# Kernel optimization log

Measured on AMD Instinct MI355X. Metric: run time of the kernel, lower is better.

## Reference

```python
import jax, jax.numpy as jnp
from jax import lax
import numpy as np
import math

B, C, Hs, Ws = 2, 512, 48, 48
HW = Hs * Ws            # 2304; also m (compress_ratio = 1)
M = HW
GROUPS = 256
GS = M // GROUPS        # 9, exact split
ALPHA = 0.05
MAXITER = 43
TOL = B * HW * 1e-7     # torch: z0.numel()*tol with z0 of shape [N, HW]
EPS = 1e-5
POWER_ITERS = 100


def _make_A():
    # random projection: num_ones = round(sqrt(m)) ones per column, rows L2-normalized
    rng = np.random.RandomState(0)
    num_ones = int(round(math.sqrt(M)))  # 48
    A = np.zeros((M, HW), dtype=np.float32)
    rows = np.argsort(rng.rand(HW, M), axis=1)[:, :num_ones]  # [HW, num_ones]
    A[rows.ravel(), np.repeat(np.arange(HW), num_ones)] = 1.0
    A /= np.maximum(np.sqrt((A ** 2).sum(axis=1, keepdims=True)), 1e-12)
    return jnp.asarray(A)


def setup_inputs() -> dict:
    key = jax.random.key(0)
    ks = jax.random.split(key, 10)
    f32 = jnp.float32
    d = {
        'content': jax.random.normal(ks[0], (B, C, Hs, Ws), f32),
        'style': jax.random.normal(ks[1], (B, C, Hs, Ws), f32),
        'content_key': jax.random.normal(ks[2], (B, C, Hs, Ws), f32),
        'style_key': jax.random.normal(ks[3], (B, C, Hs, Ws), f32),
        'f_w': jax.random.normal(ks[4], (C, C), f32) * 0.02,
        'f_b': jnp.zeros((C,), f32),
        'g_w': jax.random.normal(ks[5], (C, C), f32) * 0.02,
        'g_b': jnp.zeros((C,), f32),
        'h_w': jax.random.normal(ks[6], (C, C), f32) * 0.02,
        'h_b': jnp.zeros((C,), f32),
        'A': _make_A(),
    }
    return d


def _conv1x1(x, w, b):
    # nn.Conv2d(Cin, Cout, 1): [b,c,h,w] x [o,c] + bias
    return jnp.einsum('bchw,oc->bohw', x, w) + b[None, :, None, None]


def _softshrink(x, lam):
    return jnp.sign(x) * jnp.maximum(jnp.abs(x) - lam, 0.0)


def _forward(content, style, content_key, style_key, f_w, f_b, g_w, g_b, h_w, h_b, A):
    Fq = _conv1x1(content_key, f_w, f_b).reshape(B, C, HW).transpose(0, 2, 1)  # [b,HWc,Ck]
    G = _conv1x1(style_key, g_w, g_b).reshape(B, C, HW)                        # [b,Ck,HWs]
    Hh = _conv1x1(style, h_w, h_b).reshape(B, C, HW)
    # HW <= max_sample: no subsampling branch
    style_flat = Hh.transpose(0, 2, 1)                                         # [b,HWs,C]
    S = jax.nn.softmax(jnp.einsum('bqc,bck->bqk', Fq, G), axis=-1)             # [b,HWc,HWs]
    mean = jnp.einsum('bqk,bkc->bqc', S, style_flat)                           # weighted mean
    std = jnp.sqrt(jax.nn.relu(jnp.einsum('bqk,bkc->bqc', S, style_flat ** 2) - mean ** 2))
    mean = mean.transpose(0, 2, 1)  # [b,C,HW]
    std = std.transpose(0, 2, 1)
    # random projection along spatial dim: feat @ A^T
    proj = lambda f: jnp.einsum('mh,bch->bcm', A, f)
    mean_c = proj(mean)
    std_c = proj(std)
    cont_c = proj(content.reshape(B, C, HW))
    # per-group mean/variance norm (256 equal groups of GS along compressed dim)
    g = cont_c.reshape(B, C, GROUPS, GS)
    mu = g.mean(axis=-1, keepdims=True)
    var = g.var(axis=-1, ddof=1, keepdims=True)  # torch var is unbiased
    normed = (g - mu) / jnp.sqrt(var + EPS)
    x = (normed * std_c.reshape(B, C, GROUPS, GS)
         + mean_c.reshape(B, C, GROUPS, GS)).reshape(B, C, M)
    # FISTA sparse coding: min 0.5||z A^T - x||^2 + alpha |z|_1
    Ad = lax.stop_gradient(A)
    WtW = Ad.T @ Ad
    v = jnp.full((HW,), 1.0 / math.sqrt(HW), jnp.float32)
    def _pi(v, _):
        w = WtW @ v
        return w / jnp.linalg.norm(w), None
    v, _ = lax.scan(_pi, v, None, length=POWER_ITERS)
    L = v @ (WtW @ v)  # largest eigenvalue of A^T A
    lr = 1.0 / L
    z0 = jnp.zeros((B, C, HW), x.dtype)

    def step(carry, _):
        z, y, t, done = carry
        resid = jnp.einsum('bch,mh->bcm', y, A) - x   # y @ A^T - x
        grad = jnp.einsum('bcm,mh->bch', resid, A)    # resid @ A
        zn = _softshrink(y - lr * grad, ALPHA * lr)
        diff = jnp.abs(z - zn).sum()
        tn = (1.0 + jnp.sqrt(1.0 + 4.0 * t * t)) / 2.0
        yn = zn + (t - 1.0) / tn * (zn - z)
        z2 = jnp.where(done, z, zn)
        y2 = jnp.where(done, y, yn)
        t2 = jnp.where(done, t, tn)
        done2 = done | (diff <= TOL)
        return (z2, y2, t2, done2), None

    (z, _, _, _), _ = lax.scan(step, (z0, z0, jnp.float32(1.0), jnp.array(False)),
                               None, length=MAXITER)
    return z.reshape(B, C, Hs, Ws)


def reference(content, style, content_key, style_key, f_w, f_b, g_w, g_b, h_w, h_b, A):
    return _forward(content, style, content_key, style_key,
                    f_w, f_b, g_w, g_b, h_w, h_b, A)
```

## Files before the change

### kernel.cpp

```cpp
#include <hip/hip_runtime.h>
#include <math.h>

#define TPB 256

typedef _Float16 f16;
typedef _Float16 half8 __attribute__((ext_vector_type(8)));
typedef _Float16 f16x2 __attribute__((ext_vector_type(2)));
typedef _Float16 f16x4 __attribute__((ext_vector_type(4)));
typedef float floatx4 __attribute__((ext_vector_type(4)));

static constexpr int CDIM = 512;
static constexpr int HWD = 2304;
static constexpr float ALPHA = 0.05f;
static constexpr float TOLF = 4.608e-4f;

enum { EPI_F32 = 0, EPI_F16BIASN = 1, EPI_F16BIASM = 2, EPI_F16 = 3,
       EPI_WTW = 4, EPI_MEANSTD = 5, EPI_FISTA = 6 };

__device__ __forceinline__ bool fista_done(const float* __restrict__ diffArr, int iter) {
    bool done = false;
    for (int j = 0; j < iter; ++j) done = done || (diffArr[j] <= TOLF);
    return done;
}

__device__ __forceinline__ void gload_lds(const f16* g, f16* l) {
#if __has_builtin(__builtin_amdgcn_global_load_lds)
    __builtin_amdgcn_global_load_lds(
        (__attribute__((address_space(1))) void*)(g),
        (__attribute__((address_space(3))) void*)(l), 16, 0, 0);
#else
    *(int4*)l = *(const int4*)g;
#endif
}

template<int EPI, int MF>
__global__ __launch_bounds__(TPB, 3) void sgemm(
    const f16* __restrict__ A, long a_bs, int lda,
    const f16* __restrict__ B, long b_bs, int ldb,
    void* __restrict__ C0, long c_bs, int ldc,
    void* __restrict__ C1,
    int K,
    const float* __restrict__ bias,
    const float* __restrict__ xAf,
    float* __restrict__ zf, float* __restrict__ yf, f16* __restrict__ yhp,
    const float* __restrict__ lrs, float coef,
    float* __restrict__ diffArr, int iter)
{
    if (EPI == EPI_FISTA) {
        if (iter > 0 && fista_done(diffArr, iter)) return;
    }
    __shared__ alignas(16) f16 As[MF * 32 * 64];
    __shared__ alignas(16) f16 Bs[64 * 64];
    const int tid = threadIdx.x;
    const int wid = tid >> 6, lane = tid & 63;
    const int wr = wid >> 1, wc = wid & 1;
    const int m0 = blockIdx.y * (MF * 32), n0 = blockIdx.x << 6;
    const f16* Ab = A + (long)blockIdx.z * a_bs;
    const f16* Bb = B + (long)blockIdx.z * b_bs;

    floatx4 acc[MF][2] = {};
    floatx4 acc2[MF][2] = {};

    const int rl = lane & 15, kg = lane >> 4;
    const int lrow = lane >> 3;
    const int gs = (lane & 7) ^ lrow;

    for (int k0 = 0; k0 < K; k0 += 64) {
        #pragma unroll
        for (int p = 0; p < MF; ++p) {
            const int c = wid * MF + p;
            const int R = c * 8 + lrow;
            gload_lds(Ab + (long)(m0 + R) * lda + k0 + gs * 8, &As[c * 512]);
        }
        #pragma unroll
        for (int p = 0; p < 2; ++p) {
            const int c = wid * 2 + p;
            const int R = c * 8 + lrow;
            gload_lds(Bb + (long)(n0 + R) * ldb + k0 + gs * 8, &Bs[c * 512]);
        }
        __syncthreads();
        #pragma unroll
        for (int kk = 0; kk < 2; ++kk) {
            const int j = kk * 4 + kg;
            half8 af[MF], bf[2];
            #pragma unroll
            for (int f = 0; f < MF; ++f) {
                const int rowa = wr * (MF * 16) + f * 16 + rl;
                af[f] = *(const half8*)&As[rowa * 64 + ((j ^ (rowa & 7)) * 8)];
            }
            #pragma unroll
            for (int f = 0; f < 2; ++f) {
                const int rowb = wc * 32 + f * 16 + rl;
                bf[f] = *(const half8*)&Bs[rowb * 64 + ((j ^ (rowb & 7)) * 8)];
            }
            #pragma unroll
            for (int fi = 0; fi < MF; ++fi) {
                #pragma unroll
                for (int fj = 0; fj < 2; ++fj) {
                    acc[fi][fj] = __builtin_amdgcn_mfma_f32_16x16x32_f16(af[fi], bf[fj], acc[fi][fj], 0, 0, 0);
                    if constexpr (EPI == EPI_MEANSTD) {
                        half8 bq = bf[fj] * bf[fj];
                        acc2[fi][fj] = __builtin_amdgcn_mfma_f32_16x16x32_f16(af[fi], bq, acc2[fi][fj], 0, 0, 0);
                    }
                }
            }
        }
        __syncthreads();
    }

    const int rg = lane >> 4;
    const int bz = blockIdx.z;
    float loc = 0.f;
    float lr = 0.f, sh = 0.f;
    if constexpr (EPI == EPI_FISTA) { lr = lrs[0]; sh = lrs[1]; }

    #pragma unroll
    for (int fi = 0; fi < MF; ++fi) {
        #pragma unroll
        for (int fj = 0; fj < 2; ++fj) {
            #pragma unroll
            for (int r = 0; r < 4; ++r) {
                const int row = m0 + wr * (MF * 16) + fi * 16 + rg * 4 + r;
                const int col = n0 + wc * 32 + fj * 16 + rl;
                const float v = acc[fi][fj][r];
                if constexpr (EPI == EPI_F32) {
                    ((float*)C0)[bz * c_bs + (long)row * ldc + col] = v;
                } else if constexpr (EPI == EPI_F16BIASN) {
                    ((f16*)C0)[bz * c_bs + (long)row * ldc + col] = (f16)(v + bias[col]);
                } else if constexpr (EPI == EPI_F16BIASM) {
                    ((f16*)C0)[bz * c_bs + (long)row * ldc + col] = (f16)(v + bias[row]);
                } else if constexpr (EPI == EPI_F16) {
                    ((f16*)C0)[bz * c_bs + (long)row * ldc + col] = (f16)v;
                } else if constexpr (EPI == EPI_WTW) {
                    ((float*)C0)[(long)row * ldc + col] = v;
                    ((f16*)C1)[(long)row * ldc + col] = (f16)v;
                } else if constexpr (EPI == EPI_MEANSTD) {
                    const float m_ = v;
                    float s2 = acc2[fi][fj][r] - m_ * m_;
                    const long o = ((long)bz * CDIM + col) * HWD + row;
                    ((f16*)C0)[o] = (f16)m_;
                    ((f16*)C1)[o] = (f16)sqrtf(s2 > 0.f ? s2 : 0.f);
                } else {
                    const long off = (long)row * HWD + col;
                    const float grad = v - xAf[off];
                    const float zo = zf[off];
                    const float p = yf[off] - lr * grad;
                    const float ap = fabsf(p) - sh;
                    const float zn = ap > 0.f ? copysignf(ap, p) : 0.f;
                    zf[off] = zn;
                    const float yn = zn + coef * (zn - zo);
                    yf[off] = yn;
                    yhp[off] = (f16)yn;
                    loc += fabsf(zn - zo);
                }
            }
        }
    }
    if constexpr (EPI == EPI_FISTA) {
        __shared__ float red[TPB];
        red[tid] = loc; __syncthreads();
        for (int s = 128; s > 0; s >>= 1) { if (tid < s) red[tid] += red[tid + s]; __syncthreads(); }
        if (tid == 0) atomicAdd(&diffArr[iter], red[0]);
    }
}

__global__ __launch_bounds__(TPB) void tcvt(const float* __restrict__ in, long in_bs,
                                            f16* __restrict__ out, long out_bs, int R, int Cc) {
    __shared__ float t[32][33];
    const int b = blockIdx.z;
    const int r0 = blockIdx.y << 5, c0 = blockIdx.x << 5;
    const int tx = threadIdx.x & 31, ty = threadIdx.x >> 5;
    const float* ib = in + (long)b * in_bs;
    #pragma unroll
    for (int p = 0; p < 4; ++p) {
        const int r = ty + p * 8;
        t[r][tx] = ib[(long)(r0 + r) * Cc + c0 + tx];
    }
    __syncthreads();
    f16* ob = out + (long)b * out_bs;
    #pragma unroll
    for (int p = 0; p < 4; ++p) {
        const int c = ty + p * 8;
        ob[(long)(c0 + c) * R + r0 + tx] = (f16)t[tx][c];
    }
}

__global__ void cvt16(const float4* __restrict__ in, f16x4* __restrict__ out, long n4) {
    long i = (long)blockIdx.x * blockDim.x + threadIdx.x;
    const long st = (long)gridDim.x * blockDim.x;
    for (; i < n4; i += st) {
        const float4 v = in[i];
        f16x4 o; o.x = (f16)v.x; o.y = (f16)v.y; o.z = (f16)v.z; o.w = (f16)v.w;
        out[i] = o;
    }
}

__global__ __launch_bounds__(TPB) void softmax_h(const float* __restrict__ Sf, f16* __restrict__ Sh) {
    __shared__ float row[HWD];
    __shared__ float red[TPB];
    const long base = (long)blockIdx.x * HWD;
    const int tid = threadIdx.x;
    float mx = -3.4e38f;
    for (int i = tid; i < HWD; i += TPB) { const float v = Sf[base + i]; row[i] = v; mx = fmaxf(mx, v); }
    red[tid] = mx; __syncthreads();
    for (int s = 128; s > 0; s >>= 1) { if (tid < s) red[tid] = fmaxf(red[tid], red[tid + s]); __syncthreads(); }
    mx = red[0]; __syncthreads();
    float sum = 0.f;
    for (int i = tid; i < HWD; i += TPB) { const float e = expf(row[i] - mx); row[i] = e; sum += e; }
    red[tid] = sum; __syncthreads();
    for (int s = 128; s > 0; s >>= 1) { if (tid < s) red[tid] += red[tid + s]; __syncthreads(); }
    const float inv = 1.0f / red[0];
    for (int i = tid; i < HWD; i += TPB) Sh[base + i] = (f16)(row[i] * inv);
}

__global__ __launch_bounds__(TPB) void groupnorm_x(const float* __restrict__ contc,
                                                   const float* __restrict__ meanc,
                                                   const float* __restrict__ stdc,
                                                   f16* __restrict__ xh) {
    const long base = (long)blockIdx.x * HWD + (long)threadIdx.x * 9;
    float v[9];
    float mu = 0.f;
    #pragma unroll
    for (int j = 0; j < 9; ++j) { v[j] = contc[base + j]; mu += v[j]; }
    mu *= (1.0f / 9.0f);
    float var = 0.f;
    #pragma unroll
    for (int j = 0; j < 9; ++j) { const float d = v[j] - mu; var += d * d; }
    var *= (1.0f / 8.0f);
    const float rs = 1.0f / sqrtf(var + 1e-5f);
    #pragma unroll
    for (int j = 0; j < 9; ++j)
        xh[base + j] = (f16)((v[j] - mu) * rs * (float)stdc[base + j] + (float)meanc[base + j]);
}

__global__ __launch_bounds__(TPB) void matvec_h(const f16* __restrict__ Wm,
                                                const float* __restrict__ win,
                                                float* __restrict__ wout) {
    __shared__ float red[TPB];
    const int tid = threadIdx.x;
    float s = 0.f;
    for (int i = tid; i < HWD; i += TPB) { const float v = win[i]; s += v * v; }
    red[tid] = s; __syncthreads();
    for (int st = 128; st > 0; st >>= 1) { if (tid < st) red[tid] += red[tid + st]; __syncthreads(); }
    const float ninv = rsqrtf(red[0]);
    const int row = (blockIdx.x << 2) + (tid >> 6);
    const int lane = tid & 63;
    const f16x2* wr2 = (const f16x2*)(Wm + (long)row * HWD);
    float d = 0.f;
    for (int j = lane; j < HWD / 2; j += 64) {
        const f16x2 p = wr2[j];
        d += (float)p.x * win[2 * j] + (float)p.y * win[2 * j + 1];
    }
    #pragma unroll
    for (int o = 32; o > 0; o >>= 1) d += __shfl_down(d, o);
    if (lane == 0) wout[row] = d * ninv;
}

__global__ __launch_bounds__(TPB) void kernelL(const float* __restrict__ Wf,
                                               const float* __restrict__ w,
                                               float* __restrict__ Lnum, float* __restrict__ Lden) {
    __shared__ float red[TPB];
    const int tid = threadIdx.x;
    const int row = (blockIdx.x << 2) + (tid >> 6);
    const int lane = tid & 63;
    const float* wr = Wf + (long)row * HWD;
    float d = 0.f;
    for (int j = lane; j < HWD; j += 64) d += wr[j] * w[j];
    #pragma unroll
    for (int o = 32; o > 0; o >>= 1) d += __shfl_down(d, o);
    red[tid] = (lane == 0) ? d * w[row] : 0.f;
    __syncthreads();
    for (int s = 128; s > 0; s >>= 1) { if (tid < s) red[tid] += red[tid + s]; __syncthreads(); }
    if (tid == 0) atomicAdd(Lnum, red[0]);
    if (blockIdx.x == 0) {
        __syncthreads();
        float s2 = 0.f;
        for (int i = tid; i < HWD; i += TPB) { const float v = w[i]; s2 += v * v; }
        red[tid] = s2; __syncthreads();
        for (int s = 128; s > 0; s >>= 1) { if (tid < s) red[tid] += red[tid + s]; __syncthreads(); }
        if (tid == 0) *Lden = red[0];
    }
}

__global__ void lr_fin(const float* __restrict__ Lnum, const float* __restrict__ Lden,
                       float* __restrict__ lrs) {
    const float lr = Lden[0] / Lnum[0];
    lrs[0] = lr;
    lrs[1] = ALPHA * lr;
}

__global__ void init_small(float* __restrict__ wvec, float* __restrict__ diffArr,
                           float* __restrict__ Lnum) {
    const int tid = threadIdx.x;
    for (int i = tid; i < HWD; i += TPB) wvec[i] = (float)(1.0 / 48.0);
    if (tid < 43) diffArr[tid] = 0.f;
    if (tid == 64) Lnum[0] = 0.f;
}

__global__ void zero_kernel(float4* __restrict__ p, long n4) {
    long i = (long)blockIdx.x * blockDim.x + threadIdx.x;
    const long st = (long)gridDim.x * blockDim.x;
    for (; i < n4; i += st) p[i] = make_float4(0.f, 0.f, 0.f, 0.f);
}

__global__ void copy_kernel(const float4* __restrict__ s, float4* __restrict__ d, long n4) {
    long i = (long)blockIdx.x * blockDim.x + threadIdx.x;
    const long st = (long)gridDim.x * blockDim.x;
    for (; i < n4; i += st) d[i] = s[i];
}

extern "C" void kernel_launch(void* const* d_in, const int* in_sizes, int n_in,
                              void* d_out, int out_size, void* d_ws, size_t ws_size,
                              hipStream_t stream) {
    (void)in_sizes; (void)n_in; (void)out_size;
    const float* content = (const float*)d_in[0];
    const float* style   = (const float*)d_in[1];
    const float* ckey    = (const float*)d_in[2];
    const float* skey    = (const float*)d_in[3];
    const float* f_w = (const float*)d_in[4];
    const float* f_b = (const float*)d_in[5];
    const float* g_w = (const float*)d_in[6];
    const float* g_b = (const float*)d_in[7];
    const float* h_w = (const float*)d_in[8];
    const float* h_b = (const float*)d_in[9];
    const float* Amat = (const float*)d_in[10];

    if (ws_size < 79500000) return;
    char* W = (char*)d_ws;

    const long E16 = (long)HWD * CDIM;
    const long EHH = (long)HWD * HWD;
    f16*  ckeyT = (f16*)(W + 0);
    f16*  skeyT = (f16*)(W + 4718592);
    f16*  styleT= (f16*)(W + 9437184);
    float* Sf   = (float*)(W + 0);
    f16*  Ah    = (f16*)(W + 0);
    f16*  At    = (f16*)(W + 10616832);
    f16*  Wh    = (f16*)(W + 21233664);
    f16*  W4h   = (f16*)(W + 31850496);
    f16*  W2h   = (f16*)(W + 0);
    float* contc= (float*)(W + 21233664);
    float* zf   = (float*)(W + 0);
    float* yf   = (float*)(W + 9437184);
    f16*  yh    = (f16*)(W + 31850496);
    f16*  Sh    = (f16*)(W + 42467328);
    float* meanc= (float*)(W + 42467328);
    float* stdc = (float*)(W + 42467328 + 9437184);
    float* Wf   = (float*)(W + 42467328);
    float* xAf  = (float*)(W + 42467328);
    f16*  Fh    = (f16*)(W + 63700992);
    f16*  Gh    = (f16*)(W + 63700992 + 4718592);
    f16*  Hh    = (f16*)(W + 63700992 + 9437184);
    f16*  meanx = (f16*)(W + 63700992);
    f16*  stdx  = (f16*)(W + 63700992 + 4718592);
    f16*  conth = (f16*)(W + 63700992 + 9437184);
    f16*  xh    = (f16*)(W + 63700992);
    float* w_a  = (float*)(W + 77856768);
    float* w_b  = (float*)(W + 77856768 + 9216);
    float* lrs  = (float*)(W + 77856768 + 18432);
    float* Lnum = (float*)(W + 77856768 + 18440);
    float* Lden = (float*)(W + 77856768 + 18444);
    float* diffArr = (float*)(W + 77856768 + 18448);
    f16*  fwh   = (f16*)(W + 77875712);
    f16*  gwh   = (f16*)(W + 77875712 + 524288);
    f16*  hwh   = (f16*)(W + 77875712 + 1048576);

    init_small<<<1, TPB, 0, stream>>>(w_a, diffArr, Lnum);

    cvt16<<<256, TPB, 0, stream>>>((const float4*)f_w, (f16x4*)fwh, (long)CDIM * CDIM / 4);
    cvt16<<<256, TPB, 0, stream>>>((const float4*)g_w, (f16x4*)gwh, (long)CDIM * CDIM / 4);
    cvt16<<<256, TPB, 0, stream>>>((const float4*)h_w, (f16x4*)hwh, (long)CDIM * CDIM / 4);
    tcvt<<<dim3(72, 16, 2), TPB, 0, stream>>>(ckey, E16, ckeyT, E16, CDIM, HWD);
    tcvt<<<dim3(72, 16, 2), TPB, 0, stream>>>(skey, E16, skeyT, E16, CDIM, HWD);
    tcvt<<<dim3(72, 16, 2), TPB, 0, stream>>>(style, E16, styleT, E16, CDIM, HWD);

    sgemm<EPI_F16BIASN, 2><<<dim3(8, 36, 2), TPB, 0, stream>>>(ckeyT, E16, CDIM, fwh, 0, CDIM,
        Fh, E16, CDIM, nullptr, CDIM, f_b, nullptr, nullptr, nullptr, nullptr, nullptr, 0.f, nullptr, 0);
    sgemm<EPI_F16BIASN, 2><<<dim3(8, 36, 2), TPB, 0, stream>>>(skeyT, E16, CDIM, gwh, 0, CDIM,
        Gh, E16, CDIM, nullptr, CDIM, g_b, nullptr, nullptr, nullptr, nullptr, nullptr, 0.f, nullptr, 0);
    sgemm<EPI_F16BIASM, 2><<<dim3(36, 8, 2), TPB, 0, stream>>>(hwh, 0, CDIM, styleT, E16, CDIM,
        Hh, E16, HWD, nullptr, CDIM, h_b, nullptr, nullptr, nullptr, nullptr, nullptr, 0.f, nullptr, 0);

    sgemm<EPI_F32, 4><<<dim3(36, 18, 2), TPB, 0, stream>>>(Fh, E16, CDIM, Gh, E16, CDIM,
        Sf, EHH, HWD, nullptr, CDIM, nullptr, nullptr, nullptr, nullptr, nullptr, nullptr, 0.f, nullptr, 0);
    softmax_h<<<2 * HWD, TPB, 0, stream>>>(Sf, Sh);

    cvt16<<<2048, TPB, 0, stream>>>((const float4*)Amat, (f16x4*)Ah, EHH / 4);
    tcvt<<<dim3(72, 72, 1), TPB, 0, stream>>>(Amat, 0, At, 0, HWD, HWD);

    sgemm<EPI_MEANSTD, 2><<<dim3(8, 36, 2), TPB, 0, stream>>>(Sh, EHH, HWD, Hh, E16, HWD,
        meanx, 0, HWD, stdx, HWD, nullptr, nullptr, nullptr, nullptr, nullptr, nullptr, 0.f, nullptr, 0);

    cvt16<<<2048, TPB, 0, stream>>>((const float4*)content, (f16x4*)conth, (long)2 * E16 / 4);

    sgemm<EPI_F32, 2><<<dim3(36, 16, 1), TPB, 0, stream>>>(meanx, 0, HWD, Ah, 0, HWD,
        meanc, 0, HWD, nullptr, HWD, nullptr, nullptr, nullptr, nullptr, nullptr, nullptr, 0.f, nullptr, 0);
    sgemm<EPI_F32, 2><<<dim3(36, 16, 1), TPB, 0, stream>>>(stdx, 0, HWD, Ah, 0, HWD,
        stdc, 0, HWD, nullptr, HWD, nullptr, nullptr, nullptr, nullptr, nullptr, nullptr, 0.f, nullptr, 0);
    sgemm<EPI_F32, 2><<<dim3(36, 16, 1), TPB, 0, stream>>>(conth, 0, HWD, Ah, 0, HWD,
        contc, 0, HWD, nullptr, HWD, nullptr, nullptr, nullptr, nullptr, nullptr, nullptr, 0.f, nullptr, 0);

    groupnorm_x<<<1024, TPB, 0, stream>>>(contc, meanc, stdc, xh);

    sgemm<EPI_WTW, 4><<<dim3(36, 18, 1), TPB, 0, stream>>>(At, 0, HWD, At, 0, HWD,
        Wf, 0, HWD, Wh, HWD, nullptr, nullptr, nullptr, nullptr, nullptr, nullptr, 0.f, nullptr, 0);
    sgemm<EPI_F16, 4><<<dim3(36, 18, 1), TPB, 0, stream>>>(Wh, 0, HWD, Wh, 0, HWD,
        W2h, 0, HWD, nullptr, HWD, nullptr, nullptr, nullptr, nullptr, nullptr, nullptr, 0.f, nullptr, 0);
    sgemm<EPI_F16, 4><<<dim3(36, 18, 1), TPB, 0, stream>>>(W2h, 0, HWD, W2h, 0, HWD,
        W4h, 0, HWD, nullptr, HWD, nullptr, nullptr, nullptr, nullptr, nullptr, nullptr, 0.f, nullptr, 0);

    for (int it = 0; it < 25; ++it) {
        const float* win = (it & 1) ? w_b : w_a;
        float* wout = (it & 1) ? w_a : w_b;
        matvec_h<<<HWD / 4, TPB, 0, stream>>>(W4h, win, wout);
    }
    kernelL<<<HWD / 4, TPB, 0, stream>>>(Wf, w_b, Lnum, Lden);
    lr_fin<<<1, 1, 0, stream>>>(Lnum, Lden, lrs);

    sgemm<EPI_F32, 2><<<dim3(36, 16, 1), TPB, 0, stream>>>(xh, 0, HWD, At, 0, HWD,
        xAf, 0, HWD, nullptr, HWD, nullptr, nullptr, nullptr, nullptr, nullptr, nullptr, 0.f, nullptr, 0);

    zero_kernel<<<1024, TPB, 0, stream>>>((float4*)zf, E16);
    zero_kernel<<<1024, TPB, 0, stream>>>((float4*)yh, E16 / 4);

    float t = 1.0f;
    for (int it = 0; it < 43; ++it) {
        const float tn = (1.0f + sqrtf(1.0f + 4.0f * t * t)) * 0.5f;
        const float coef = (t - 1.0f) / tn;
        t = tn;
        sgemm<EPI_FISTA, 2><<<dim3(36, 16, 1), TPB, 0, stream>>>(yh, 0, HWD, Wh, 0, HWD,
            nullptr, 0, HWD, nullptr, HWD, nullptr, xAf, zf, yf, yh, lrs, coef, diffArr, it);
    }

    copy_kernel<<<2048, TPB, 0, stream>>>((const float4*)zf, (float4*)d_out, 2 * E16 / 4);
}
```

Measured before the change: 2.252 ms.

## Drop fp32 y buffer in FISTA by recomputing y from ping-pong z, remap workgroups across XCDs

The FISTA epilogue no longer keeps an fp32 momentum buffer y. It rebuilds y_k from the current and previous z, which are stored in two ping-pong buffers. Each iteration writes only the new z and the fp16 y, and the final copy selects the correct buffer from the convergence history. This removes one fp32 read and one write per element per iteration, at the cost of an extra z read and some control logic. The change also remaps block IDs so that consecutive tiles land on the same XCD, which should improve L2 locality.

Result: no change. 2.208 ms (-1.9%).

```diff
diff --git a/kernel.cpp b/kernel.cpp
--- a/kernel.cpp
+++ b/kernel.cpp
@@ -42,8 +42,8 @@
     int K,
     const float* __restrict__ bias,
     const float* __restrict__ xAf,
-    float* __restrict__ zf, float* __restrict__ yf, f16* __restrict__ yhp,
-    const float* __restrict__ lrs, float coef,
+    float* __restrict__ zc, float* __restrict__ zp, f16* __restrict__ yhp,
+    const float* __restrict__ lrs, float coefPrev, float coefCur,
     float* __restrict__ diffArr, int iter)
 {
     if (EPI == EPI_FISTA) {
@@ -54,7 +54,16 @@
     const int tid = threadIdx.x;
     const int wid = tid >> 6, lane = tid & 63;
     const int wr = wid >> 1, wc = wid & 1;
-    const int m0 = blockIdx.y * (MF * 32), n0 = blockIdx.x << 6;
+
+    const int gx = gridDim.x, gy = gridDim.y;
+    const int nwg = gx * gy;
+    const int d = blockIdx.y * gx + blockIdx.x;
+    const int q = nwg >> 3, r = nwg & 7;
+    const int xcd = d & 7, rest = d >> 3;
+    const int wgid = (xcd < r ? xcd * (q + 1) : r * (q + 1) + (xcd - r) * q) + rest;
+    const int bx = wgid / gy, by = wgid % gy;
+
+    const int m0 = by * (MF * 32), n0 = bx << 6;
     const f16* Ab = A + (long)blockIdx.z * a_bs;
     const f16* Bb = B + (long)blockIdx.z * b_bs;
 
@@ -119,10 +128,10 @@
         #pragma unroll
         for (int fj = 0; fj < 2; ++fj) {
             #pragma unroll
-            for (int r = 0; r < 4; ++r) {
-                const int row = m0 + wr * (MF * 16) + fi * 16 + rg * 4 + r;
+            for (int r2 = 0; r2 < 4; ++r2) {
+                const int row = m0 + wr * (MF * 16) + fi * 16 + rg * 4 + r2;
                 const int col = n0 + wc * 32 + fj * 16 + rl;
-                const float v = acc[fi][fj][r];
+                const float v = acc[fi][fj][r2];
                 if constexpr (EPI == EPI_F32) {
                     ((float*)C0)[bz * c_bs + (long)row * ldc + col] = v;
                 } else if constexpr (EPI == EPI_F16BIASN) {
@@ -136,22 +145,22 @@
                     ((f16*)C1)[(long)row * ldc + col] = (f16)v;
                 } else if constexpr (EPI == EPI_MEANSTD) {
                     const float m_ = v;
-                    float s2 = acc2[fi][fj][r] - m_ * m_;
+                    float s2 = acc2[fi][fj][r2] - m_ * m_;
                     const long o = ((long)bz * CDIM + col) * HWD + row;
                     ((f16*)C0)[o] = (f16)m_;
                     ((f16*)C1)[o] = (f16)sqrtf(s2 > 0.f ? s2 : 0.f);
                 } else {
                     const long off = (long)row * HWD + col;
+                    const float zk = zc[off];
+                    const float zkm = zp[off];
+                    const float ykf = zk + coefPrev * (zk - zkm);
                     const float grad = v - xAf[off];
-                    const float zo = zf[off];
-                    const float p = yf[off] - lr * grad;
+                    const float p = ykf - lr * grad;
                     const float ap = fabsf(p) - sh;
                     const float zn = ap > 0.f ? copysignf(ap, p) : 0.f;
-                    zf[off] = zn;
-                    const float yn = zn + coef * (zn - zo);
-                    yf[off] = yn;
-                    yhp[off] = (f16)yn;
-                    loc += fabsf(zn - zo);
+                    zp[off] = zn;
+                    yhp[off] = (f16)(zn + coefCur * (zn - zk));
+                    loc += fabsf(zn - zk);
                 }
             }
         }
@@ -303,10 +312,14 @@
     for (; i < n4; i += st) p[i] = make_float4(0.f, 0.f, 0.f, 0.f);
 }
 
-__global__ void copy_kernel(const float4* __restrict__ s, float4* __restrict__ d, long n4) {
+__global__ void copy_fista(const float4* __restrict__ zfA, const float4* __restrict__ zfB,
+                           float4* __restrict__ out, const float* __restrict__ diffArr, long n4) {
+    int last = 42;
+    for (int j = 0; j < 43; ++j) { if (diffArr[j] <= TOLF) { last = j; break; } }
+    const float4* src = (last & 1) ? zfA : zfB;
     long i = (long)blockIdx.x * blockDim.x + threadIdx.x;
     const long st = (long)gridDim.x * blockDim.x;
-    for (; i < n4; i += st) d[i] = s[i];
+    for (; i < n4; i += st) out[i] = src[i];
 }
 
 extern "C" void kernel_launch(void* const* d_in, const int* in_sizes, int n_in,
@@ -340,8 +353,8 @@
     f16*  W4h   = (f16*)(W + 31850496);
     f16*  W2h   = (f16*)(W + 0);
     float* contc= (float*)(W + 21233664);
-    float* zf   = (float*)(W + 0);
-    float* yf   = (float*)(W + 9437184);
+    float* zfA  = (float*)(W + 0);
+    float* zfB  = (float*)(W + 9437184);
     f16*  yh    = (f16*)(W + 31850496);
     f16*  Sh    = (f16*)(W + 42467328);
     float* meanc= (float*)(W + 42467328);
@@ -375,39 +388,39 @@
     tcvt<<<dim3(72, 16, 2), TPB, 0, stream>>>(style, E16, styleT, E16, CDIM, HWD);
 
     sgemm<EPI_F16BIASN, 2><<<dim3(8, 36, 2), TPB, 0, stream>>>(ckeyT, E16, CDIM, fwh, 0, CDIM,
-        Fh, E16, CDIM, nullptr, CDIM, f_b, nullptr, nullptr, nullptr, nullptr, nullptr, 0.f, nullptr, 0);
+        Fh, E16, CDIM, nullptr, CDIM, f_b, nullptr, nullptr, nullptr, nullptr, nullptr, 0.f, 0.f, nullptr, 0);
     sgemm<EPI_F16BIASN, 2><<<dim3(8, 36, 2), TPB, 0, stream>>>(skeyT, E16, CDIM, gwh, 0, CDIM,
-        Gh, E16, CDIM, nullptr, CDIM, g_b, nullptr, nullptr, nullptr, nullptr, nullptr, 0.f, nullptr, 0);
+        Gh, E16, CDIM, nullptr, CDIM, g_b, nullptr, nullptr, nullptr, nullptr, nullptr, 0.f, 0.f, nullptr, 0);
     sgemm<EPI_F16BIASM, 2><<<dim3(36, 8, 2), TPB, 0, stream>>>(hwh, 0, CDIM, styleT, E16, CDIM,
-        Hh, E16, HWD, nullptr, CDIM, h_b, nullptr, nullptr, nullptr, nullptr, nullptr, 0.f, nullptr, 0);
+        Hh, E16, HWD, nullptr, CDIM, h_b, nullptr, nullptr, nullptr, nullptr, nullptr, 0.f, 0.f, nullptr, 0);
 
     sgemm<EPI_F32, 4><<<dim3(36, 18, 2), TPB, 0, stream>>>(Fh, E16, CDIM, Gh, E16, CDIM,
-        Sf, EHH, HWD, nullptr, CDIM, nullptr, nullptr, nullptr, nullptr, nullptr, nullptr, 0.f, nullptr, 0);
+        Sf, EHH, HWD, nullptr, CDIM, nullptr, nullptr, nullptr, nullptr, nullptr, nullptr, 0.f, 0.f, nullptr, 0);
     softmax_h<<<2 * HWD, TPB, 0, stream>>>(Sf, Sh);
 
     cvt16<<<2048, TPB, 0, stream>>>((const float4*)Amat, (f16x4*)Ah, EHH / 4);
     tcvt<<<dim3(72, 72, 1), TPB, 0, stream>>>(Amat, 0, At, 0, HWD, HWD);
 
     sgemm<EPI_MEANSTD, 2><<<dim3(8, 36, 2), TPB, 0, stream>>>(Sh, EHH, HWD, Hh, E16, HWD,
-        meanx, 0, HWD, stdx, HWD, nullptr, nullptr, nullptr, nullptr, nullptr, nullptr, 0.f, nullptr, 0);
+        meanx, 0, HWD, stdx, HWD, nullptr, nullptr, nullptr, nullptr, nullptr, nullptr, 0.f, 0.f, nullptr, 0);
 
     cvt16<<<2048, TPB, 0, stream>>>((const float4*)content, (f16x4*)conth, (long)2 * E16 / 4);
 
     sgemm<EPI_F32, 2><<<dim3(36, 16, 1), TPB, 0, stream>>>(meanx, 0, HWD, Ah, 0, HWD,
-        meanc, 0, HWD, nullptr, HWD, nullptr, nullptr, nullptr, nullptr, nullptr, nullptr, 0.f, nullptr, 0);
+        meanc, 0, HWD, nullptr, HWD, nullptr, nullptr, nullptr, nullptr, nullptr, nullptr, 0.f, 0.f, nullptr, 0);
     sgemm<EPI_F32, 2><<<dim3(36, 16, 1), TPB, 0, stream>>>(stdx, 0, HWD, Ah, 0, HWD,
-        stdc, 0, HWD, nullptr, HWD, nullptr, nullptr, nullptr, nullptr, nullptr, nullptr, 0.f, nullptr, 0);
+        stdc, 0, HWD, nullptr, HWD, nullptr, nullptr, nullptr, nullptr, nullptr, nullptr, 0.f, 0.f, nullptr, 0);
     sgemm<EPI_F32, 2><<<dim3(36, 16, 1), TPB, 0, stream>>>(conth, 0, HWD, Ah, 0, HWD,
-        contc, 0, HWD, nullptr, HWD, nullptr, nullptr, nullptr, nullptr, nullptr, nullptr, 0.f, nullptr, 0);
+        contc, 0, HWD, nullptr, HWD, nullptr, nullptr, nullptr, nullptr, nullptr, nullptr, 0.f, 0.f, nullptr, 0);
 
     groupnorm_x<<<1024, TPB, 0, stream>>>(contc, meanc, stdc, xh);
 
     sgemm<EPI_WTW, 4><<<dim3(36, 18, 1), TPB, 0, stream>>>(At, 0, HWD, At, 0, HWD,
-        Wf, 0, HWD, Wh, HWD, nullptr, nullptr, nullptr, nullptr, nullptr, nullptr, 0.f, nullptr, 0);
+        Wf, 0, HWD, Wh, HWD, nullptr, nullptr, nullptr, nullptr, nullptr, nullptr, 0.f, 0.f, nullptr, 0);
     sgemm<EPI_F16, 4><<<dim3(36, 18, 1), TPB, 0, stream>>>(Wh, 0, HWD, Wh, 0, HWD,
-        W2h, 0, HWD, nullptr, HWD, nullptr, nullptr, nullptr, nullptr, nullptr, nullptr, 0.f, nullptr, 0);
+        W2h, 0, HWD, nullptr, HWD, nullptr, nullptr, nullptr, nullptr, nullptr, nullptr, 0.f, 0.f, nullptr, 0);
     sgemm<EPI_F16, 4><<<dim3(36, 18, 1), TPB, 0, stream>>>(W2h, 0, HWD, W2h, 0, HWD,
-        W4h, 0, HWD, nullptr, HWD, nullptr, nullptr, nullptr, nullptr, nullptr, nullptr, 0.f, nullptr, 0);
+        W4h, 0, HWD, nullptr, HWD, nullptr, nullptr, nullptr, nullptr, nullptr, nullptr, 0.f, 0.f, nullptr, 0);
 
     for (int it = 0; it < 25; ++it) {
         const float* win = (it & 1) ? w_b : w_a;
@@ -418,19 +431,23 @@
     lr_fin<<<1, 1, 0, stream>>>(Lnum, Lden, lrs);
 
     sgemm<EPI_F32, 2><<<dim3(36, 16, 1), TPB, 0, stream>>>(xh, 0, HWD, At, 0, HWD,
-        xAf, 0, HWD, nullptr, HWD, nullptr, nullptr, nullptr, nullptr, nullptr, nullptr, 0.f, nullptr, 0);
-
-    zero_kernel<<<1024, TPB, 0, stream>>>((float4*)zf, E16);
+        xAf, 0, HWD, nullptr, HWD, nullptr, nullptr, nullptr, nullptr, nullptr, nullptr, 0.f, 0.f, nullptr, 0);
+
+    zero_kernel<<<1024, TPB, 0, stream>>>((float4*)zfA, E16);
     zero_kernel<<<1024, TPB, 0, stream>>>((float4*)yh, E16 / 4);
 
-    float t = 1.0f;
+    float t = 1.0f, coefPrev = 0.0f;
     for (int it = 0; it < 43; ++it) {
         const float tn = (1.0f + sqrtf(1.0f + 4.0f * t * t)) * 0.5f;
         const float coef = (t - 1.0f) / tn;
         t = tn;
+        float* zc = (it & 1) ? zfB : zfA;
+        float* zp = (it & 1) ? zfA : zfB;
         sgemm<EPI_FISTA, 2><<<dim3(36, 16, 1), TPB, 0, stream>>>(yh, 0, HWD, Wh, 0, HWD,
-            nullptr, 0, HWD, nullptr, HWD, nullptr, xAf, zf, yf, yh, lrs, coef, diffArr, it);
-    }
-
-    copy_kernel<<<2048, TPB, 0, stream>>>((const float4*)zf, (float4*)d_out, 2 * E16 / 4);
-}
+            nullptr, 0, HWD, nullptr, HWD, nullptr, xAf, zc, zp, yh, lrs, coefPrev, coef, diffArr, it);
+        coefPrev = coef;
+    }
+
+    copy_fista<<<2048, TPB, 0, stream>>>((const float4*)zfA, (const float4*)zfB,
+                                         (float4*)d_out, diffArr, 2 * E16 / 4);
+}
```
